# Kernel optimization log

Measured on AMD Instinct MI355X. Metric: run time of the kernel, lower is better.

The kernel has to match this reference:

```python
import jax, jax.numpy as jnp
import numpy as np

D = 1024
H = 16
HD = D // H  # 64


def setup_inputs() -> dict:
    key = jax.random.key(0)
    ks = jax.random.split(key, 11)
    B, L = 2, 2048
    std = 0.02
    return {
        "query": jax.random.normal(ks[0], (B, L, D), jnp.float32),
        "key": jax.random.normal(ks[1], (B, L, D), jnp.float32),
        "value": jax.random.normal(ks[2], (B, L, D), jnp.float32),
        "Wq": jax.random.normal(ks[3], (D, D), jnp.float32) * std,
        "bq": jnp.zeros((D,), jnp.float32),
        "Wk": jax.random.normal(ks[4], (D, D), jnp.float32) * std,
        "bk": jnp.zeros((D,), jnp.float32),
        "Wv": jax.random.normal(ks[5], (D, D), jnp.float32) * std,
        "bv": jnp.zeros((D,), jnp.float32),
        "Wo": jax.random.normal(ks[6], (D, D), jnp.float32) * std,
        "bo": jnp.zeros((D,), jnp.float32),
    }


def _split_heads(x):
    # [B, L, D] -> [B, H, L, HD]
    B, L, _ = x.shape
    return x.reshape(B, L, H, HD).transpose(0, 2, 1, 3)


def reference(query, key, value, Wq, bq, Wk, bk, Wv, bv, Wo, bo):
    B, Lq, _ = query.shape
    # Linear projections (torch Linear: x @ W.T + b)
    Q = _split_heads(query @ Wq.T + bq)
    K = _split_heads(key @ Wk.T + bk)
    V = _split_heads(value @ Wv.T + bv)
    scale = HD ** -0.5
    scores = jnp.einsum("bhqd,bhkd->bhqk", Q, K) * scale  # [B,H,Lq,Lk]
    weights = jax.nn.softmax(scores, axis=-1)
    attended = jnp.einsum("bhqk,bhkd->bhqd", weights, V)  # [B,H,Lq,HD]
    attended = attended.transpose(0, 2, 1, 3).reshape(B, Lq, D)
    output = attended @ Wo.T + bo
    return output, weights.mean(axis=1)
```

## Files before the change

### kernel.cpp

```cpp
#include <hip/hip_runtime.h>
#include <stdint.h>

#define D_MODEL 1024
#define NHEAD 16
#define HDIM 64
#define SEQ 2048
#define NTOK 4096
#define KVB 128
#define NT (KVB / 16)
#define PSTR 136

typedef unsigned short u16;
typedef float f32x4 __attribute__((ext_vector_type(4)));
typedef __bf16 bf16x8 __attribute__((ext_vector_type(8)));
typedef unsigned int u32x4 __attribute__((ext_vector_type(4)));
typedef u16 u16x4 __attribute__((ext_vector_type(4)));

#define QSC 0.180336880111117f

__device__ __forceinline__ u16 fcast_bf(float f) {
  __bf16 h = (__bf16)f;
  return __builtin_bit_cast(u16, h);
}

__device__ __forceinline__ float exp2_fast(float x) {
#if __has_builtin(__builtin_amdgcn_exp2f)
  return __builtin_amdgcn_exp2f(x);
#else
  return __expf(x * 0.69314718056f);
#endif
}

__device__ __forceinline__ bf16x8 scale_q(bf16x8 q) {
  bf16x8 r;
#pragma unroll
  for (int i = 0; i < 8; i++) r[i] = (__bf16)((float)q[i] * QSC);
  return r;
}

__device__ __forceinline__ bf16x8 lds_frag(const u16* sm, int off) {
  return *reinterpret_cast<const bf16x8*>(sm + off);
}

__device__ __forceinline__ void gload_lds16(const u16* g, u16* l) {
  __builtin_amdgcn_global_load_lds((const __attribute__((address_space(1))) void*)g,
                                   (__attribute__((address_space(3))) void*)l, 16, 0, 0);
}

__global__ void cvt3_kernel(const float* __restrict__ s0, const float* __restrict__ s1,
                            const float* __restrict__ s2, u16* __restrict__ dst, int n4) {
  const float* s = blockIdx.y == 0 ? s0 : (blockIdx.y == 1 ? s1 : s2);
  u16* d = dst + (size_t)blockIdx.y * n4 * 4;
  int i = blockIdx.x * blockDim.x + threadIdx.x;
  int stride = gridDim.x * blockDim.x;
  for (; i < n4; i += stride) {
    f32x4 v = reinterpret_cast<const f32x4*>(s)[i];
    u16x4 o;
    o[0] = fcast_bf(v[0]); o[1] = fcast_bf(v[1]);
    o[2] = fcast_bf(v[2]); o[3] = fcast_bf(v[3]);
    reinterpret_cast<u16x4*>(d)[i] = o;
  }
}

__global__ void cvt4_kernel(const float* __restrict__ s0, const float* __restrict__ s1,
                            const float* __restrict__ s2, const float* __restrict__ s3,
                            u16* __restrict__ dst, int n4) {
  const float* s = blockIdx.y == 0 ? s0 : (blockIdx.y == 1 ? s1 : (blockIdx.y == 2 ? s2 : s3));
  u16* d = dst + (size_t)blockIdx.y * n4 * 4;
  int i = blockIdx.x * blockDim.x + threadIdx.x;
  int stride = gridDim.x * blockDim.x;
  for (; i < n4; i += stride) {
    f32x4 v = reinterpret_cast<const f32x4*>(s)[i];
    u16x4 o;
    o[0] = fcast_bf(v[0]); o[1] = fcast_bf(v[1]);
    o[2] = fcast_bf(v[2]); o[3] = fcast_bf(v[3]);
    reinterpret_cast<u16x4*>(d)[i] = o;
  }
}

template<int MODE>
__global__ __launch_bounds__(256)
void gemm_kernel(const u16* __restrict__ Abase, const u16* __restrict__ Wbase,
                 const float* __restrict__ b0, const float* __restrict__ b1,
                 const float* __restrict__ b2,
                 u16* __restrict__ obf, float* __restrict__ of32) {
  const int z = (MODE == 0) ? blockIdx.z : 0;
  const u16* A = Abase + (size_t)z * NTOK * D_MODEL;
  const u16* W = Wbase + (size_t)z * D_MODEL * D_MODEL;
  const float* bias = (MODE == 0) ? (z == 0 ? b0 : (z == 1 ? b1 : b2)) : b0;
  u16* oz = (MODE == 0) ? (obf + (size_t)z * NTOK * D_MODEL) : obf;

  const int bn0 = blockIdx.x * 128;
  const int bm0 = blockIdx.y * 128;
  const int tid = threadIdx.x;
  const int lane = tid & 63, wid = tid >> 6;
  const int wm = wid >> 1, wn = wid & 1;
  const int l15 = lane & 15, l4 = lane >> 4;
  const int lrow8 = lane >> 3, lch = lane & 7;

  __shared__ u16 smA[128 * 64];
  __shared__ u16 smB[128 * 64];

  f32x4 acc[4][4];
#pragma unroll
  for (int mi = 0; mi < 4; mi++)
#pragma unroll
    for (int ni = 0; ni < 4; ni++) acc[mi][ni] = f32x4{0.f, 0.f, 0.f, 0.f};

  for (int it = 0; it < D_MODEL / 64; it++) {
    const int k0 = it * 64;
    __syncthreads();
#pragma unroll
    for (int c2 = 0; c2 < 4; c2++) {
      int blk = wid * 4 + c2;
      int base16 = blk * 512;
      int row = blk * 8 + lrow8;
      gload_lds16(A + (size_t)(bm0 + row) * D_MODEL + k0 + lch * 8, &smA[base16]);
      gload_lds16(W + (size_t)(bn0 + row) * D_MODEL + k0 + lch * 8, &smB[base16]);
    }
    __syncthreads();
#pragma unroll
    for (int kk = 0; kk < 2; kk++) {
      bf16x8 af[4], bfv[4];
#pragma unroll
      for (int mi = 0; mi < 4; mi++) {
        int r = wm * 64 + mi * 16 + l15;
        af[mi] = lds_frag(smA, r * 64 + (kk * 4 + l4) * 8);
      }
#pragma unroll
      for (int ni = 0; ni < 4; ni++) {
        int r = wn * 64 + ni * 16 + l15;
        bfv[ni] = lds_frag(smB, r * 64 + (kk * 4 + l4) * 8);
      }
#pragma unroll
      for (int mi = 0; mi < 4; mi++)
#pragma unroll
        for (int ni = 0; ni < 4; ni++)
          acc[mi][ni] = __builtin_amdgcn_mfma_f32_16x16x32_bf16(af[mi], bfv[ni], acc[mi][ni], 0, 0, 0);
    }
  }

#pragma unroll
  for (int mi = 0; mi < 4; mi++) {
#pragma unroll
    for (int ni = 0; ni < 4; ni++) {
      int colg = bn0 + wn * 64 + ni * 16 + l15;
      float bv = bias[colg];
      if (MODE == 0 && z == 2) {
        int h = colg >> 6, hd = colg & 63;
        int row0 = bm0 + wm * 64 + mi * 16 + l4 * 4;
        int b = row0 >> 11, lq = row0 & 2047;
        u16x4 pk;
#pragma unroll
        for (int j = 0; j < 4; j++) pk[j] = fcast_bf(acc[mi][ni][j] + bv);
        size_t idx = ((size_t)((b * NHEAD + h) * HDIM + hd)) * SEQ + lq;
        *reinterpret_cast<u16x4*>(oz + idx) = pk;
      } else {
#pragma unroll
        for (int j = 0; j < 4; j++) {
          int rowg = bm0 + wm * 64 + mi * 16 + l4 * 4 + j;
          float v = acc[mi][ni][j] + bv;
          if (MODE == 0) {
            int b = rowg >> 11, lq = rowg & 2047;
            int h = colg >> 6, hd = colg & 63;
            oz[((size_t)((b * NHEAD + h) * SEQ + lq)) * HDIM + hd] = fcast_bf(v);
          } else {
            of32[(size_t)rowg * D_MODEL + colg] = v;
          }
        }
      }
    }
  }
}

__global__ __launch_bounds__(256)
void attn_kernel(const u16* __restrict__ Qh, const u16* __restrict__ Kh,
                 const u16* __restrict__ Vh, u16* __restrict__ attb,
                 float* __restrict__ m_ws, float* __restrict__ linv_ws) {
  const int qt0 = blockIdx.x * 64;
  const int bh = blockIdx.y;
  const int b = bh >> 4, h = bh & 15;
  const int tid = threadIdx.x;
  const int lane = tid & 63, wid = tid >> 6;
  const int l15 = lane & 15, l4 = lane >> 4;

  const u16* Qp = Qh + (size_t)bh * SEQ * HDIM;
  const u16* Kp = Kh + (size_t)bh * SEQ * HDIM;
  const u16* Vp = Vh + (size_t)bh * HDIM * SEQ;

  __shared__ u16 smK[KVB * 64];
  __shared__ u16 smV[64 * KVB];
  __shared__ u16 smP[4][16 * PSTR];

  bf16x8 qf[2];
  {
    const u16* qrow = Qp + (size_t)(qt0 + wid * 16 + l15) * HDIM;
    qf[0] = scale_q(*reinterpret_cast<const bf16x8*>(qrow + l4 * 8));
    qf[1] = scale_q(*reinterpret_cast<const bf16x8*>(qrow + 32 + l4 * 8));
  }

  float m = -1e30f, lsum = 0.f;
  f32x4 oacc[4];
#pragma unroll
  for (int d = 0; d < 4; d++) oacc[d] = f32x4{0.f, 0.f, 0.f, 0.f};

  u32x4 rk[4], rv[4];
#pragma unroll
  for (int i = 0; i < 4; i++) {
    int c = i * 256 + tid;
    rk[i] = *reinterpret_cast<const u32x4*>(Kp + (size_t)(c >> 3) * HDIM + (c & 7) * 8);
    rv[i] = *reinterpret_cast<const u32x4*>(Vp + (size_t)(c >> 4) * SEQ + (c & 15) * 8);
  }

  for (int kt = 0; kt < SEQ / KVB; kt++) {
    __syncthreads();
#pragma unroll
    for (int i = 0; i < 4; i++) {
      int c = i * 256 + tid;
      { int row = c >> 3, ch = c & 7;
        *reinterpret_cast<u32x4*>(&smK[row * 64 + ((ch ^ (row & 7)) * 8)]) = rk[i]; }
      { int row = c >> 4, ch = c & 15;
        *reinterpret_cast<u32x4*>(&smV[row * KVB + ((ch ^ (row & 15)) * 8)]) = rv[i]; }
    }
    __syncthreads();
    if (kt + 1 < SEQ / KVB) {
      int kn = (kt + 1) * KVB;
#pragma unroll
      for (int i = 0; i < 4; i++) {
        int c = i * 256 + tid;
        rk[i] = *reinterpret_cast<const u32x4*>(Kp + (size_t)(kn + (c >> 3)) * HDIM + (c & 7) * 8);
        rv[i] = *reinterpret_cast<const u32x4*>(Vp + (size_t)(c >> 4) * SEQ + kn + (c & 15) * 8);
      }
    }
    f32x4 s[NT];
#pragma unroll
    for (int nt = 0; nt < NT; nt++) s[nt] = f32x4{0.f, 0.f, 0.f, 0.f};
#pragma unroll
    for (int kk = 0; kk < 2; kk++) {
#pragma unroll
      for (int nt = 0; nt < NT; nt++) {
        int r = nt * 16 + l15;
        int ch = (kk * 4 + l4) ^ (r & 7);
        bf16x8 kf = lds_frag(smK, r * 64 + ch * 8);
        s[nt] = __builtin_amdgcn_mfma_f32_16x16x32_bf16(kf, qf[kk], s[nt], 0, 0, 0);
      }
    }
    float smax = s[0][0];
#pragma unroll
    for (int nt = 0; nt < NT; nt++)
#pragma unroll
      for (int j = 0; j < 4; j++) smax = fmaxf(smax, s[nt][j]);
    smax = fmaxf(smax, __shfl_xor(smax, 16));
    smax = fmaxf(smax, __shfl_xor(smax, 32));
    float mn = fmaxf(m, smax);
    float corr = exp2_fast(m - mn);
    m = mn;
#pragma unroll
    for (int d = 0; d < 4; d++)
#pragma unroll
      for (int j = 0; j < 4; j++) oacc[d][j] *= corr;
    float ps = 0.f;
#pragma unroll
    for (int nt = 0; nt < NT; nt++) {
      u16x4 pwv;
#pragma unroll
      for (int j = 0; j < 4; j++) {
        float pv = exp2_fast(s[nt][j] - mn);
        ps += pv;
        pwv[j] = fcast_bf(pv);
      }
      *reinterpret_cast<u16x4*>(&smP[wid][l15 * PSTR + nt * 16 + l4 * 4]) = pwv;
    }
    ps += __shfl_xor(ps, 16);
    ps += __shfl_xor(ps, 32);
    lsum = lsum * corr + ps;
#pragma unroll
    for (int kc = 0; kc < 4; kc++) {
      bf16x8 pf = lds_frag(smP[wid], l15 * PSTR + kc * 32 + l4 * 8);
#pragma unroll
      for (int d = 0; d < 4; d++) {
        int r = d * 16 + l15;
        int ch = (kc * 4 + l4) ^ (r & 15);
        bf16x8 vf = lds_frag(smV, r * KVB + ch * 8);
        oacc[d] = __builtin_amdgcn_mfma_f32_16x16x32_bf16(vf, pf, oacc[d], 0, 0, 0);
      }
    }
  }

  const float li = 1.f / lsum;
  const int token = qt0 + wid * 16 + l15;
  if (l4 == 0) {
    m_ws[(size_t)bh * SEQ + token] = m;
    linv_ws[(size_t)bh * SEQ + token] = li;
  }
#pragma unroll
  for (int d = 0; d < 4; d++) {
    u16x4 pk;
#pragma unroll
    for (int j = 0; j < 4; j++) pk[j] = fcast_bf(oacc[d][j] * li);
    *reinterpret_cast<u16x4*>(
        attb + ((size_t)(b * SEQ + token)) * D_MODEL + h * HDIM + d * 16 + l4 * 4) = pk;
  }
}

__global__ __launch_bounds__(256)
void mean_kernel(const u16* __restrict__ Qh, const u16* __restrict__ Kh,
                 const float* __restrict__ m_ws, const float* __restrict__ linv_ws,
                 float* __restrict__ out1) {
  const int kt0 = blockIdx.x * 64;
  const int qt0 = blockIdx.y * 64;
  const int b = blockIdx.z;
  const int tid = threadIdx.x;
  const int lane = tid & 63, wid = tid >> 6;
  const int l15 = lane & 15, l4 = lane >> 4;

  __shared__ u16 smK[64 * 64];

  f32x4 macc[4];
#pragma unroll
  for (int nt = 0; nt < 4; nt++) macc[nt] = f32x4{0.f, 0.f, 0.f, 0.f};

  const int rbase = qt0 + wid * 16 + l4 * 4;
  const size_t qoff = (size_t)(qt0 + wid * 16 + l15) * HDIM;

  u32x4 rk[2];
  bf16x8 qfa, qfb;
  {
    const u16* Kp0 = Kh + (size_t)(b * NHEAD) * SEQ * HDIM;
#pragma unroll
    for (int i = 0; i < 2; i++) {
      int c = i * 256 + tid;
      rk[i] = *reinterpret_cast<const u32x4*>(Kp0 + (size_t)(kt0 + (c >> 3)) * HDIM + (c & 7) * 8);
    }
    const u16* Qp0 = Qh + (size_t)(b * NHEAD) * SEQ * HDIM + qoff;
    qfa = scale_q(*reinterpret_cast<const bf16x8*>(Qp0 + l4 * 8));
    qfb = scale_q(*reinterpret_cast<const bf16x8*>(Qp0 + 32 + l4 * 8));
  }

  for (int h = 0; h < NHEAD; h++) {
    const int bh = b * NHEAD + h;
    __syncthreads();
#pragma unroll
    for (int i = 0; i < 2; i++) {
      int c = i * 256 + tid;
      int row = c >> 3, ch = c & 7;
      *reinterpret_cast<u32x4*>(&smK[row * 64 + ((ch ^ (row & 7)) * 8)]) = rk[i];
    }
    __syncthreads();
    u32x4 rkn[2];
    bf16x8 qfan, qfbn;
    if (h + 1 < NHEAD) {
      const u16* Kp1 = Kh + (size_t)(bh + 1) * SEQ * HDIM;
#pragma unroll
      for (int i = 0; i < 2; i++) {
        int c = i * 256 + tid;
        rkn[i] = *reinterpret_cast<const u32x4*>(Kp1 + (size_t)(kt0 + (c >> 3)) * HDIM + (c & 7) * 8);
      }
      const u16* Qp1 = Qh + (size_t)(bh + 1) * SEQ * HDIM + qoff;
      qfan = scale_q(*reinterpret_cast<const bf16x8*>(Qp1 + l4 * 8));
      qfbn = scale_q(*reinterpret_cast<const bf16x8*>(Qp1 + 32 + l4 * 8));
    }
    f32x4 s[4];
#pragma unroll
    for (int nt = 0; nt < 4; nt++) s[nt] = f32x4{0.f, 0.f, 0.f, 0.f};
#pragma unroll
    for (int kk = 0; kk < 2; kk++) {
#pragma unroll
      for (int nt = 0; nt < 4; nt++) {
        int r = nt * 16 + l15;
        int ch = (kk * 4 + l4) ^ (r & 7);
        bf16x8 kf = lds_frag(smK, r * 64 + ch * 8);
        s[nt] = __builtin_amdgcn_mfma_f32_16x16x32_bf16(kk == 0 ? qfa : qfb, kf, s[nt], 0, 0, 0);
      }
    }
    f32x4 mv = *reinterpret_cast<const f32x4*>(&m_ws[(size_t)bh * SEQ + rbase]);
    f32x4 lv = *reinterpret_cast<const f32x4*>(&linv_ws[(size_t)bh * SEQ + rbase]);
#pragma unroll
    for (int nt = 0; nt < 4; nt++)
#pragma unroll
      for (int j = 0; j < 4; j++)
        macc[nt][j] += exp2_fast(s[nt][j] - mv[j]) * lv[j];
    if (h + 1 < NHEAD) {
      rk[0] = rkn[0]; rk[1] = rkn[1];
      qfa = qfan; qfb = qfbn;
    }
  }
  const float invh = 1.f / 16.f;
#pragma unroll
  for (int nt = 0; nt < 4; nt++)
#pragma unroll
    for (int j = 0; j < 4; j++)
      out1[((size_t)(b * SEQ + rbase + j)) * SEQ + kt0 + nt * 16 + l15] = macc[nt][j] * invh;
}

extern "C" void kernel_launch(void* const* d_in, const int* in_sizes, int n_in,
                              void* d_out, int out_size, void* d_ws, size_t ws_size,
                              hipStream_t stream) {
  (void)in_sizes; (void)n_in; (void)out_size; (void)ws_size;
  const float* query = (const float*)d_in[0];
  const float* key = (const float*)d_in[1];
  const float* value = (const float*)d_in[2];
  const float* Wq = (const float*)d_in[3];
  const float* bq = (const float*)d_in[4];
  const float* Wk = (const float*)d_in[5];
  const float* bk = (const float*)d_in[6];
  const float* Wv = (const float*)d_in[7];
  const float* bv = (const float*)d_in[8];
  const float* Wo = (const float*)d_in[9];
  const float* bo = (const float*)d_in[10];

  char* ws = (char*)d_ws;
  u16* xb = (u16*)(ws);
  u16* wb = (u16*)(ws + 25165824);
  u16* Qhp = (u16*)(ws + 33554432);
  u16* attb = (u16*)(ws + 58720256);
  float* m_ws = (float*)(ws + 67108864);
  float* linv_ws = (float*)(ws + 67371008);

  float* out0 = (float*)d_out;
  float* out1 = out0 + (size_t)NTOK * D_MODEL;

  cvt3_kernel<<<dim3(512, 3), 256, 0, stream>>>(query, key, value, xb, 1048576);
  cvt4_kernel<<<dim3(192, 4), 256, 0, stream>>>(Wq, Wk, Wv, Wo, wb, 262144);

  gemm_kernel<0><<<dim3(8, 32, 3), 256, 0, stream>>>(xb, wb, bq, bk, bv, Qhp, nullptr);
  attn_kernel<<<dim3(32, 32), 256, 0, stream>>>(Qhp, Qhp + 4194304, Qhp + 8388608,
                                                attb, m_ws, linv_ws);
  mean_kernel<<<dim3(32, 32, 2), 256, 0, stream>>>(Qhp, Qhp + 4194304, m_ws, linv_ws, out1);
  gemm_kernel<1><<<dim3(8, 32, 1), 256, 0, stream>>>(attb, wb + 3 * 1048576, bo, bo, bo,
                                                     nullptr, out0);
}
```

Measured before the change: 227.7 us.

## Swizzle GEMM block order, XOR-swizzle attention P buffer, widen mean-kernel blocks

The GEMM remaps its flat block index so that consecutive blocks walk down M within an N column, which is meant to improve L2 reuse of the weight tiles. The attention kernel replaces the padded P scratch buffer with an XOR-swizzled unpadded layout to cut LDS footprint and bank conflicts, and moves the output rescale after the P writes. The mean kernel goes to 512 threads covering 128 query rows per block, so each K tile staged in LDS is reused by twice as many query rows. The larger blocks may reduce occupancy or add register pressure.

```diff
diff --git a/kernel.cpp b/kernel.cpp
--- a/kernel.cpp
+++ b/kernel.cpp
@@ -8,7 +8,6 @@
 #define NTOK 4096
 #define KVB 128
 #define NT (KVB / 16)
-#define PSTR 136
 
 typedef unsigned short u16;
 typedef float f32x4 __attribute__((ext_vector_type(4)));
@@ -90,8 +89,10 @@
   const float* bias = (MODE == 0) ? (z == 0 ? b0 : (z == 1 ? b1 : b2)) : b0;
   u16* oz = (MODE == 0) ? (obf + (size_t)z * NTOK * D_MODEL) : obf;
 
-  const int bn0 = blockIdx.x * 128;
-  const int bm0 = blockIdx.y * 128;
+  const int flat = blockIdx.y * 8 + blockIdx.x;
+  const int nf = (flat & 7) * 32 + (flat >> 3);
+  const int bn0 = (nf & 7) * 128;
+  const int bm0 = (nf >> 3) * 128;
   const int tid = threadIdx.x;
   const int lane = tid & 63, wid = tid >> 6;
   const int wm = wid >> 1, wn = wid & 1;
@@ -190,7 +191,7 @@
 
   __shared__ u16 smK[KVB * 64];
   __shared__ u16 smV[64 * KVB];
-  __shared__ u16 smP[4][16 * PSTR];
+  __shared__ u16 smP[4][16 * KVB];
 
   bf16x8 qf[2];
   {
@@ -255,10 +256,6 @@
     float mn = fmaxf(m, smax);
     float corr = exp2_fast(m - mn);
     m = mn;
-#pragma unroll
-    for (int d = 0; d < 4; d++)
-#pragma unroll
-      for (int j = 0; j < 4; j++) oacc[d][j] *= corr;
     float ps = 0.f;
 #pragma unroll
     for (int nt = 0; nt < NT; nt++) {
@@ -269,14 +266,20 @@
         ps += pv;
         pwv[j] = fcast_bf(pv);
       }
-      *reinterpret_cast<u16x4*>(&smP[wid][l15 * PSTR + nt * 16 + l4 * 4]) = pwv;
+      int sp = (nt * 4 + l4) ^ (l15 * 2);
+      *reinterpret_cast<u16x4*>(&smP[wid][l15 * KVB + sp * 4]) = pwv;
     }
     ps += __shfl_xor(ps, 16);
     ps += __shfl_xor(ps, 32);
     lsum = lsum * corr + ps;
 #pragma unroll
+    for (int d = 0; d < 4; d++)
+#pragma unroll
+      for (int j = 0; j < 4; j++) oacc[d][j] *= corr;
+#pragma unroll
     for (int kc = 0; kc < 4; kc++) {
-      bf16x8 pf = lds_frag(smP[wid], l15 * PSTR + kc * 32 + l4 * 8);
+      int chp = (kc * 4 + l4) ^ l15;
+      bf16x8 pf = lds_frag(smP[wid], l15 * KVB + chp * 8);
 #pragma unroll
       for (int d = 0; d < 4; d++) {
         int r = d * 16 + l15;
@@ -303,12 +306,12 @@
   }
 }
 
-__global__ __launch_bounds__(256)
+__global__ __launch_bounds__(512)
 void mean_kernel(const u16* __restrict__ Qh, const u16* __restrict__ Kh,
                  const float* __restrict__ m_ws, const float* __restrict__ linv_ws,
                  float* __restrict__ out1) {
   const int kt0 = blockIdx.x * 64;
-  const int qt0 = blockIdx.y * 64;
+  const int qt0 = blockIdx.y * 128;
   const int b = blockIdx.z;
   const int tid = threadIdx.x;
   const int lane = tid & 63, wid = tid >> 6;
@@ -323,15 +326,11 @@
   const int rbase = qt0 + wid * 16 + l4 * 4;
   const size_t qoff = (size_t)(qt0 + wid * 16 + l15) * HDIM;
 
-  u32x4 rk[2];
+  u32x4 rk;
   bf16x8 qfa, qfb;
   {
     const u16* Kp0 = Kh + (size_t)(b * NHEAD) * SEQ * HDIM;
-#pragma unroll
-    for (int i = 0; i < 2; i++) {
-      int c = i * 256 + tid;
-      rk[i] = *reinterpret_cast<const u32x4*>(Kp0 + (size_t)(kt0 + (c >> 3)) * HDIM + (c & 7) * 8);
-    }
+    rk = *reinterpret_cast<const u32x4*>(Kp0 + (size_t)(kt0 + (tid >> 3)) * HDIM + (tid & 7) * 8);
     const u16* Qp0 = Qh + (size_t)(b * NHEAD) * SEQ * HDIM + qoff;
     qfa = scale_q(*reinterpret_cast<const bf16x8*>(Qp0 + l4 * 8));
     qfb = scale_q(*reinterpret_cast<const bf16x8*>(Qp0 + 32 + l4 * 8));
@@ -340,22 +339,16 @@
   for (int h = 0; h < NHEAD; h++) {
     const int bh = b * NHEAD + h;
     __syncthreads();
-#pragma unroll
-    for (int i = 0; i < 2; i++) {
-      int c = i * 256 + tid;
-      int row = c >> 3, ch = c & 7;
-      *reinterpret_cast<u32x4*>(&smK[row * 64 + ((ch ^ (row & 7)) * 8)]) = rk[i];
-    }
-    __syncthreads();
-    u32x4 rkn[2];
+    {
+      int row = tid >> 3, ch = tid & 7;
+      *reinterpret_cast<u32x4*>(&smK[row * 64 + ((ch ^ (row & 7)) * 8)]) = rk;
+    }
+    __syncthreads();
+    u32x4 rkn;
     bf16x8 qfan, qfbn;
     if (h + 1 < NHEAD) {
       const u16* Kp1 = Kh + (size_t)(bh + 1) * SEQ * HDIM;
-#pragma unroll
-      for (int i = 0; i < 2; i++) {
-        int c = i * 256 + tid;
-        rkn[i] = *reinterpret_cast<const u32x4*>(Kp1 + (size_t)(kt0 + (c >> 3)) * HDIM + (c & 7) * 8);
-      }
+      rkn = *reinterpret_cast<const u32x4*>(Kp1 + (size_t)(kt0 + (tid >> 3)) * HDIM + (tid & 7) * 8);
       const u16* Qp1 = Qh + (size_t)(bh + 1) * SEQ * HDIM + qoff;
       qfan = scale_q(*reinterpret_cast<const bf16x8*>(Qp1 + l4 * 8));
       qfbn = scale_q(*reinterpret_cast<const bf16x8*>(Qp1 + 32 + l4 * 8));
@@ -381,7 +374,7 @@
       for (int j = 0; j < 4; j++)
         macc[nt][j] += exp2_fast(s[nt][j] - mv[j]) * lv[j];
     if (h + 1 < NHEAD) {
-      rk[0] = rkn[0]; rk[1] = rkn[1];
+      rk = rkn;
       qfa = qfan; qfb = qfbn;
     }
   }
@@ -426,7 +419,7 @@
   gemm_kernel<0><<<dim3(8, 32, 3), 256, 0, stream>>>(xb, wb, bq, bk, bv, Qhp, nullptr);
   attn_kernel<<<dim3(32, 32), 256, 0, stream>>>(Qhp, Qhp + 4194304, Qhp + 8388608,
                                                 attb, m_ws, linv_ws);
-  mean_kernel<<<dim3(32, 32, 2), 256, 0, stream>>>(Qhp, Qhp + 4194304, m_ws, linv_ws, out1);
+  mean_kernel<<<dim3(32, 16, 2), 512, 0, stream>>>(Qhp, Qhp + 4194304, m_ws, linv_ws, out1);
   gemm_kernel<1><<<dim3(8, 32, 1), 256, 0, stream>>>(attb, wb + 3 * 1048576, bo, bo, bo,
                                                      nullptr, out0);
 }
```

Result: no change. 226.3 us (-0.6%).
